# Optimization experiments

Measured on AMD Instinct MI355X. Metric: run time of the kernel, lower is better.

The kernel has to match this reference:

```python
import jax, jax.numpy as jnp
import numpy as np

V, H, HALF, L, B = 32000, 512, 256, 1024, 64
LN_EPS = 1e-5
DELTA_EPS = 1e-6


def _forward(seq, embed, ff_w1, ff_b1, ff_w2, ff_b2, ln_g, ln_b,
             sem_w, sem_b, epi_w, epi_b, out_w, out_b):
    # Encoder: embed -> residual FFN -> LayerNorm
    e = embed[seq]                                   # (B, L, H)
    ff = jax.nn.relu(e @ ff_w1 + ff_b1) @ ff_w2 + ff_b2
    x = e + ff
    mu = jnp.mean(x, axis=-1, keepdims=True)
    var = jnp.mean((x - mu) ** 2, axis=-1, keepdims=True)
    h = (x - mu) / jnp.sqrt(var + LN_EPS) * ln_g + ln_b  # (B, L, H)

    # Project all timesteps at once (batched GEMM instead of per-step Linear)
    ks_all = h @ sem_w + sem_b                       # (B, L, half)
    ke_all = h @ epi_w + epi_b                       # (B, L, half)

    Bsz = seq.shape[0]
    Ls = seq.shape[1]
    w_t = jnp.arange(1, Ls, dtype=h.dtype) / Ls      # (L-1,) linear recency weights

    def step(carry, inp):
        M_s, M_e = carry
        k_s, k_e, w = inp                            # (B, half), (B, half), scalar
        vps = jnp.einsum('bij,bj->bi', M_s, k_s)
        dvs = k_s - vps / (jnp.sum(k_s * k_s, axis=-1, keepdims=True) + DELTA_EPS)
        M_s = M_s + dvs[:, :, None] * k_s[:, None, :]
        vpe = jnp.einsum('bij,bj->bi', M_e, k_e)
        dve = k_e - vpe / (jnp.sum(k_e * k_e, axis=-1, keepdims=True) + DELTA_EPS)
        M_e = M_e + w * (dve[:, :, None] * k_e[:, None, :])
        return (M_s, M_e), None

    M0 = jnp.zeros((Bsz, HALF, HALF), dtype=h.dtype)
    xs = (jnp.swapaxes(ks_all[:, :-1], 0, 1),        # (L-1, B, half)
          jnp.swapaxes(ke_all[:, :-1], 0, 1),
          w_t)
    (M_s, M_e), _ = jax.lax.scan(step, (M0, M0), xs)

    cs = jnp.einsum('bij,bj->bi', M_s, ks_all[:, -1])
    ce = jnp.einsum('bij,bj->bi', M_e, ke_all[:, -1])
    return jnp.concatenate([cs, ce], axis=-1) @ out_w + out_b  # (B, V)


def setup_inputs() -> dict:
    key = jax.random.key(0)
    ks = jax.random.split(key, 8)
    n = lambda k, shape, s=0.02: jax.random.normal(k, shape, jnp.float32) * s
    return {
        'seq': jax.random.randint(ks[0], (B, L), 0, V),
        'embed': n(ks[1], (V, H)),
        'ff_w1': n(ks[2], (H, 2 * H)), 'ff_b1': jnp.zeros((2 * H,), jnp.float32),
        'ff_w2': n(ks[3], (2 * H, H)), 'ff_b2': jnp.zeros((H,), jnp.float32),
        'ln_g': jnp.ones((H,), jnp.float32), 'ln_b': jnp.zeros((H,), jnp.float32),
        'sem_w': n(ks[4], (H, HALF)), 'sem_b': jnp.zeros((HALF,), jnp.float32),
        'epi_w': n(ks[5], (H, HALF)), 'epi_b': jnp.zeros((HALF,), jnp.float32),
        'out_w': n(ks[6], (2 * HALF, V)), 'out_b': jnp.zeros((V,), jnp.float32),
    }


def reference(seq, embed, ff_w1, ff_b1, ff_w2, ff_b2, ln_g, ln_b,
              sem_w, sem_b, epi_w, epi_b, out_w, out_b):
    return _forward(seq, embed, ff_w1, ff_b1, ff_w2, ff_b2, ln_g, ln_b,
                    sem_w, sem_b, epi_w, epi_b, out_w, out_b)
```

## Files before the change

### kernel.cpp

```cpp
#include <hip/hip_runtime.h>

typedef unsigned short ushort_t;
typedef unsigned int uint_t;
typedef __attribute__((ext_vector_type(8))) short short8;
typedef __attribute__((ext_vector_type(4))) float f32x4;

static constexpr int V = 32000, H = 512, HALFD = 256, LSEQ = 1024, BB = 64;

__device__ __forceinline__ ushort_t f2bf(float f) {
    uint_t u = __float_as_uint(f);
    u = (u + 0x7FFFu + ((u >> 16) & 1u)) >> 16;
    return (ushort_t)u;
}
__device__ __forceinline__ float bf2f(ushort_t u) {
    return __uint_as_float(((uint_t)u) << 16);
}
__device__ __forceinline__ float bflo(uint_t u) { return __uint_as_float(u << 16); }
__device__ __forceinline__ float bfhi(uint_t u) { return __uint_as_float(u & 0xffff0000u); }

__global__ void transpose_cvt(const float* __restrict__ W, ushort_t* __restrict__ Wt,
                              int K, int N) {
    __shared__ float tile[32][33];
    int k0 = blockIdx.y * 32, n0 = blockIdx.x * 32;
    int tx = threadIdx.x & 31, ty = threadIdx.x >> 5;
    #pragma unroll
    for (int i = 0; i < 32; i += 8)
        tile[ty + i][tx] = W[(size_t)(k0 + ty + i) * N + n0 + tx];
    __syncthreads();
    #pragma unroll
    for (int i = 0; i < 32; i += 8)
        Wt[(size_t)(n0 + ty + i) * K + k0 + tx] = f2bf(tile[tx][ty + i]);
}

__global__ __launch_bounds__(512) void enc_fused(
        const int* __restrict__ seqp, const float* __restrict__ embed,
        const ushort_t* __restrict__ W1t, const ushort_t* __restrict__ W2t,
        const float* __restrict__ b1, const float* __restrict__ b2,
        const float* __restrict__ lng, const float* __restrict__ lnb,
        const ushort_t* __restrict__ Pt,
        const float* __restrict__ biasS, const float* __restrict__ biasE,
        ushort_t* __restrict__ outS, ushort_t* __restrict__ outE,
        float* __restrict__ bet_s, float* __restrict__ bet_e) {
    __shared__ __align__(16) ushort_t El[64 * 520];
    __shared__ __align__(16) ushort_t T1l[64 * 264];
    __shared__ __align__(16) ushort_t Bst[512 * 40];
    __shared__ int toks[64];
    __shared__ float lnP[64 * 8], lnQ[64 * 8];
    __shared__ float lnM[64], lnR[64];

    int t = threadIdx.x;
    int lane = t & 63, w = t >> 6;
    int lid = lane & 15, quad = lane >> 4;
    int m0 = blockIdx.x * 64;

    if (t < 64) toks[t] = seqp[m0 + t];
    {
        int r = t >> 3, c0 = (t & 7) * 64;
        const float* e = embed + (size_t)seqp[m0 + r] * H + c0;
        #pragma unroll
        for (int j = 0; j < 8; ++j) {
            float4 a = *(const float4*)(e + j * 8);
            float4 bq = *(const float4*)(e + j * 8 + 4);
            short8 sv;
            sv[0] = (short)f2bf(a.x);  sv[1] = (short)f2bf(a.y);
            sv[2] = (short)f2bf(a.z);  sv[3] = (short)f2bf(a.w);
            sv[4] = (short)f2bf(bq.x); sv[5] = (short)f2bf(bq.y);
            sv[6] = (short)f2bf(bq.z); sv[7] = (short)f2bf(bq.w);
            *(short8*)&El[r * 520 + c0 + j * 8] = sv;
        }
    }

    f32x4 acc2[4][4];
    #pragma unroll
    for (int i = 0; i < 4; ++i)
        #pragma unroll
        for (int j = 0; j < 4; ++j)
            acc2[i][j] = (f32x4){0.f, 0.f, 0.f, 0.f};
    __syncthreads();

    for (int s = 0; s < 4; ++s) {
        f32x4 acc1[4][2];
        #pragma unroll
        for (int i = 0; i < 4; ++i)
            #pragma unroll
            for (int j = 0; j < 2; ++j)
                acc1[i][j] = (f32x4){0.f, 0.f, 0.f, 0.f};
        for (int kc = 0; kc < 16; ++kc) {
            {
                int r = t >> 1, ko = (t & 1) * 16;
                const ushort_t* src = W1t + (size_t)(s * 256 + r) * 512 + kc * 32 + ko;
                *(short8*)&Bst[r * 40 + ko]     = *(const short8*)(src);
                *(short8*)&Bst[r * 40 + ko + 8] = *(const short8*)(src + 8);
            }
            __syncthreads();
            short8 af[4], bfr[2];
            #pragma unroll
            for (int i = 0; i < 4; ++i)
                af[i] = *(const short8*)&El[(i * 16 + lid) * 520 + kc * 32 + quad * 8];
            #pragma unroll
            for (int i = 0; i < 2; ++i)
                bfr[i] = *(const short8*)&Bst[(w * 32 + i * 16 + lid) * 40 + quad * 8];
            #pragma unroll
            for (int mt = 0; mt < 4; ++mt)
                #pragma unroll
                for (int nt = 0; nt < 2; ++nt)
                    acc1[mt][nt] = __builtin_amdgcn_mfma_f32_16x16x32_bf16(
                        af[mt], bfr[nt], acc1[mt][nt], 0, 0, 0);
            __syncthreads();
        }
        #pragma unroll
        for (int mt = 0; mt < 4; ++mt)
            #pragma unroll
            for (int nt = 0; nt < 2; ++nt) {
                int col = w * 32 + nt * 16 + lid;
                float bc = b1[s * 256 + col];
                #pragma unroll
                for (int rg = 0; rg < 4; ++rg) {
                    int row = mt * 16 + quad * 4 + rg;
                    T1l[row * 264 + col] = f2bf(fmaxf(acc1[mt][nt][rg] + bc, 0.f));
                }
            }
        for (int kc = 0; kc < 8; ++kc) {
            {
                const ushort_t* src = W2t + (size_t)t * 1024 + s * 256 + kc * 32;
                #pragma unroll
                for (int j = 0; j < 4; ++j)
                    *(short8*)&Bst[t * 40 + j * 8] = *(const short8*)(src + j * 8);
            }
            __syncthreads();
            short8 af[4], bfr[4];
            #pragma unroll
            for (int i = 0; i < 4; ++i)
                af[i] = *(const short8*)&T1l[(i * 16 + lid) * 264 + kc * 32 + quad * 8];
            #pragma unroll
            for (int i = 0; i < 4; ++i)
                bfr[i] = *(const short8*)&Bst[(w * 64 + i * 16 + lid) * 40 + quad * 8];
            #pragma unroll
            for (int mt = 0; mt < 4; ++mt)
                #pragma unroll
                for (int nt = 0; nt < 4; ++nt)
                    acc2[mt][nt] = __builtin_amdgcn_mfma_f32_16x16x32_bf16(
                        af[mt], bfr[nt], acc2[mt][nt], 0, 0, 0);
            __syncthreads();
        }
    }

    #pragma unroll
    for (int mt = 0; mt < 4; ++mt)
        #pragma unroll
        for (int rg = 0; rg < 4; ++rg) {
            int row = mt * 16 + quad * 4 + rg;
            const float* er = embed + (size_t)toks[row] * H;
            #pragma unroll
            for (int nt = 0; nt < 4; ++nt) {
                int col = w * 64 + nt * 16 + lid;
                acc2[mt][nt][rg] += b2[col] + er[col];
            }
        }
    #pragma unroll
    for (int mt = 0; mt < 4; ++mt)
        #pragma unroll
        for (int rg = 0; rg < 4; ++rg) {
            float sv = 0.f, qv = 0.f;
            #pragma unroll
            for (int nt = 0; nt < 4; ++nt) {
                float v = acc2[mt][nt][rg];
                sv += v; qv += v * v;
            }
            #pragma unroll
            for (int d = 1; d < 16; d <<= 1) {
                sv += __shfl_xor(sv, d);
                qv += __shfl_xor(qv, d);
            }
            int row = mt * 16 + quad * 4 + rg;
            if (lid == 0) { lnP[row * 8 + w] = sv; lnQ[row * 8 + w] = qv; }
        }
    __syncthreads();
    if (t < 64) {
        float sv = 0.f, qv = 0.f;
        #pragma unroll
        for (int j = 0; j < 8; ++j) { sv += lnP[t * 8 + j]; qv += lnQ[t * 8 + j]; }
        float mu = sv * (1.f / 512.f);
        float var = qv * (1.f / 512.f) - mu * mu;
        lnM[t] = mu;
        lnR[t] = rsqrtf(var + 1e-5f);
    }
    __syncthreads();
    #pragma unroll
    for (int mt = 0; mt < 4; ++mt)
        #pragma unroll
        for (int rg = 0; rg < 4; ++rg) {
            int row = mt * 16 + quad * 4 + rg;
            float mu = lnM[row], rs = lnR[row];
            #pragma unroll
            for (int nt = 0; nt < 4; ++nt) {
                int col = w * 64 + nt * 16 + lid;
                El[row * 520 + col] =
                    f2bf((acc2[mt][nt][rg] - mu) * rs * lng[col] + lnb[col]);
            }
        }
    __syncthreads();

    f32x4 acc3[4][4];
    #pragma unroll
    for (int i = 0; i < 4; ++i)
        #pragma unroll
        for (int j = 0; j < 4; ++j)
            acc3[i][j] = (f32x4){0.f, 0.f, 0.f, 0.f};
    for (int kc = 0; kc < 16; ++kc) {
        {
            const ushort_t* src = Pt + (size_t)t * 512 + kc * 32;
            #pragma unroll
            for (int j = 0; j < 4; ++j)
                *(short8*)&Bst[t * 40 + j * 8] = *(const short8*)(src + j * 8);
        }
        __syncthreads();
        short8 af[4], bfr[4];
        #pragma unroll
        for (int i = 0; i < 4; ++i)
            af[i] = *(const short8*)&El[(i * 16 + lid) * 520 + kc * 32 + quad * 8];
        #pragma unroll
        for (int i = 0; i < 4; ++i)
            bfr[i] = *(const short8*)&Bst[(w * 64 + i * 16 + lid) * 40 + quad * 8];
        #pragma unroll
        for (int mt = 0; mt < 4; ++mt)
            #pragma unroll
            for (int nt = 0; nt < 4; ++nt)
                acc3[mt][nt] = __builtin_amdgcn_mfma_f32_16x16x32_bf16(
                    af[mt], bfr[nt], acc3[mt][nt], 0, 0, 0);
        __syncthreads();
    }
    {
        const float* bb = (w < 4) ? (biasS + w * 64) : (biasE + (w - 4) * 64);
        ushort_t* op = (w < 4) ? outS : outE;
        int cbase = (w < 4) ? (w * 64) : ((w - 4) * 64);
        #pragma unroll
        for (int mt = 0; mt < 4; ++mt)
            #pragma unroll
            for (int rg = 0; rg < 4; ++rg) {
                int row = mt * 16 + quad * 4 + rg;
                float sq = 0.f;
                #pragma unroll
                for (int nt = 0; nt < 4; ++nt) {
                    int c = nt * 16 + lid;
                    ushort_t hv = f2bf(acc3[mt][nt][rg] + bb[c]);
                    op[(size_t)(m0 + row) * HALFD + cbase + c] = hv;
                    float fv = bf2f(hv);
                    sq += fv * fv;
                }
                #pragma unroll
                for (int d = 1; d < 16; d <<= 1) sq += __shfl_xor(sq, d);
                if (lid == 0) lnP[row * 8 + w] = sq;
            }
        __syncthreads();
        if (t < 128) {
            int row = t & 63;
            int w0 = (t < 64) ? 0 : 4;
            float sv = lnP[row * 8 + w0] + lnP[row * 8 + w0 + 1]
                     + lnP[row * 8 + w0 + 2] + lnP[row * 8 + w0 + 3];
            float* bout = (t < 64) ? bet_s : bet_e;
            bout[m0 + row] = sv + 1e-6f;
        }
    }
}

__global__ __launch_bounds__(256) void tinv_kernel(
        const ushort_t* __restrict__ ks, const ushort_t* __restrict__ ke,
        const float* __restrict__ beta_s, const float* __restrict__ beta_e,
        ushort_t* __restrict__ Dg) {
    __shared__ __align__(16) ushort_t Kl[64][280];
    __shared__ __align__(16) ushort_t LmT[4][64][66];
    __shared__ float betsl[4][64];

    int t = threadIdx.x;
    int lane = t & 63, wv = t >> 6;
    int lid = lane & 15, quad = lane >> 4;
    int blk0 = blockIdx.x * 4;
    const float invL = 1.0f / 1024.0f;

    for (int pp = 0; pp < 4; ++pp) {
        int p = blk0 + pp;
        int ch = p & 15, bm = p >> 4;
        int mat = bm & 1, b = bm >> 1;
        const ushort_t* Kp = (mat ? ke : ks) + ((size_t)b * LSEQ + ch * 64) * HALFD;
        const float* Bp = (mat ? beta_e : beta_s) + (size_t)b * LSEQ + ch * 64;

        __syncthreads();
        {
            int j = t >> 2, c0 = (t & 3) * 64;
            const ushort_t* src = Kp + (size_t)j * HALFD + c0;
            #pragma unroll
            for (int x = 0; x < 8; ++x)
                *(short8*)&Kl[j][c0 + x * 8] = *(const short8*)(src + x * 8);
        }
        if (t < 64) betsl[pp][t] = Bp[t];
        __syncthreads();

        f32x4 g[4];
        #pragma unroll
        for (int i = 0; i < 4; ++i) g[i] = (f32x4){0.f, 0.f, 0.f, 0.f};
        #pragma unroll
        for (int kc = 0; kc < 8; ++kc) {
            short8 af = *(const short8*)&Kl[wv * 16 + lid][kc * 32 + quad * 8];
            #pragma unroll
            for (int nt = 0; nt < 4; ++nt) {
                short8 bq = *(const short8*)&Kl[nt * 16 + lid][kc * 32 + quad * 8];
                g[nt] = __builtin_amdgcn_mfma_f32_16x16x32_bf16(af, bq, g[nt], 0, 0, 0);
            }
        }
        #pragma unroll
        for (int nt = 0; nt < 4; ++nt)
            #pragma unroll
            for (int rg = 0; rg < 4; ++rg) {
                int i = wv * 16 + quad * 4 + rg;
                int j = nt * 16 + lid;
                int s = ch * 64 + i;
                float wgt = mat ? (float)(s + 1) * invL : 1.0f;
                if (s >= 1023) wgt = 0.f;
                float wb = wgt / betsl[pp][i];
                LmT[pp][j][i] = f2bf((j < i) ? g[nt][rg] * wb : 0.f);
            }
    }
    __syncthreads();

    const ushort_t (*Lp)[66] = LmT[wv];
    float a[64];
    #pragma unroll
    for (int x = 0; x < 32; ++x) {
        uint_t u = *(const uint_t*)&Lp[lane][x * 2];
        a[x * 2]     = -bflo(u);
        a[x * 2 + 1] = -bfhi(u);
    }
    #pragma unroll
    for (int j = 0; j < 63; ++j) {
        float dj = a[j];
        const ushort_t* rowj = Lp[j];
        #pragma unroll
        for (int ii = (j + 1) & ~1; ii < 64; ii += 2) {
            uint_t u = *(const uint_t*)&rowj[ii];
            if (ii > j) a[ii] -= bflo(u) * dj;
            a[ii + 1]        -= bfhi(u) * dj;
        }
    }
    size_t pbase = (size_t)(blk0 + wv) * 4096;
    #pragma unroll
    for (int i = 0; i < 64; ++i)
        Dg[pbase + (size_t)i * 64 + lane] = f2bf(a[i]);
}

__global__ __launch_bounds__(512) void scan_kernel(
        const ushort_t* __restrict__ ks, const ushort_t* __restrict__ ke,
        const float* __restrict__ beta_s, const float* __restrict__ beta_e,
        const ushort_t* __restrict__ Dg, float* __restrict__ c) {
    int blk = blockIdx.x;
    int b = blk >> 2, mat = (blk >> 1) & 1, half = blk & 1;
    const ushort_t* Kp = (mat ? ke : ks) + (size_t)b * LSEQ * HALFD;
    const float* Bp = (mat ? beta_e : beta_s) + (size_t)b * LSEQ;
    const ushort_t* Dp = Dg + (size_t)(b * 2 + mat) * 16 * 4096;

    __shared__ __align__(16) ushort_t Kl[64][264];
    __shared__ __align__(16) ushort_t MK[33792];
    __shared__ __align__(16) ushort_t RHSl[128][72];
    __shared__ __align__(16) ushort_t Ul[128][72];
    __shared__ __align__(16) ushort_t Dl[64][72];
    __shared__ float bets[LSEQ];

    ushort_t (*Ml)[264] = (ushort_t(*)[264])MK;
    ushort_t (*Kt)[72]  = (ushort_t(*)[72])MK;

    int t = threadIdx.x;
    int lane = t & 63, wid = t >> 6;
    int lid = lane & 15, quad = lane >> 4;
    int wm  = (wid & 1) * 64, wn  = (wid >> 1) * 64;
    int wm1 = (wid & 1) * 64, wn1 = (wid >> 1) * 16;

    #pragma unroll
    for (int i = 0; i < 2; ++i) bets[t + i * 512] = Bp[t + i * 512];

    f32x4 acc[4][4];
    #pragma unroll
    for (int i = 0; i < 4; ++i)
        #pragma unroll
        for (int j = 0; j < 4; ++j)
            acc[i][j] = (f32x4){0.f, 0.f, 0.f, 0.f};

    int sj = t >> 3, scb = (t & 7) * 8;
    short8 pf[4];
    {
        const ushort_t* kr = Kp + (size_t)sj * HALFD + scb;
        #pragma unroll
        for (int x = 0; x < 4; ++x) pf[x] = *(const short8*)(kr + x * 64);
    }
    short8 dpf = *(const short8*)(Dp + t * 8);
    const float invL = 1.0f / 1024.0f;

    for (int ch = 0; ch < 16; ++ch) {
        __syncthreads();
        #pragma unroll
        for (int x = 0; x < 4; ++x) *(short8*)&Kl[sj][scb + x * 64] = pf[x];
        *(short8*)&Dl[t >> 3][(t & 7) * 8] = dpf;
        #pragma unroll
        for (int mt = 0; mt < 4; ++mt)
            #pragma unroll
            for (int nt = 0; nt < 4; ++nt)
                #pragma unroll
                for (int rg = 0; rg < 4; ++rg)
                    Ml[wm + mt * 16 + quad * 4 + rg][wn + nt * 16 + lid] =
                        f2bf(acc[mt][nt][rg]);
        int nch = (ch + 1 < 16) ? ch + 1 : 15;
        {
            const ushort_t* kr = Kp + ((size_t)nch * 64 + sj) * HALFD + scb;
            #pragma unroll
            for (int x = 0; x < 4; ++x) pf[x] = *(const short8*)(kr + x * 64);
            dpf = *(const short8*)(Dp + (size_t)nch * 4096 + t * 8);
        }
        __syncthreads();

        f32x4 p0[4];
        #pragma unroll
        for (int i = 0; i < 4; ++i) p0[i] = (f32x4){0.f, 0.f, 0.f, 0.f};
        #pragma unroll
        for (int kc = 0; kc < 8; ++kc) {
            short8 bq = *(const short8*)&Kl[wn1 + lid][kc * 32 + quad * 8];
            #pragma unroll
            for (int mt = 0; mt < 4; ++mt) {
                short8 aq = *(const short8*)&Ml[wm1 + mt * 16 + lid][kc * 32 + quad * 8];
                p0[mt] = __builtin_amdgcn_mfma_f32_16x16x32_bf16(aq, bq, p0[mt], 0, 0, 0);
            }
        }
        __syncthreads();
        #pragma unroll
        for (int mt = 0; mt < 4; ++mt)
            #pragma unroll
            for (int nt = 0; nt < 4; ++nt)
                #pragma unroll
                for (int rg = 0; rg < 4; ++rg) {
                    float v = acc[mt][nt][rg];
                    Ml[wm + mt * 16 + quad * 4 + rg][wn + nt * 16 + lid] =
                        f2bf(v - bf2f(f2bf(v)));
                }
        __syncthreads();
        #pragma unroll
        for (int kc = 0; kc < 8; ++kc) {
            short8 bq = *(const short8*)&Kl[wn1 + lid][kc * 32 + quad * 8];
            #pragma unroll
            for (int mt = 0; mt < 4; ++mt) {
                short8 aq = *(const short8*)&Ml[wm1 + mt * 16 + lid][kc * 32 + quad * 8];
                p0[mt] = __builtin_amdgcn_mfma_f32_16x16x32_bf16(aq, bq, p0[mt], 0, 0, 0);
            }
        }
        int iB = wn1 + lid;
        int s = ch * 64 + iB;
        float wgt = mat ? (float)(s + 1) * invL : 1.0f;
        if (s >= 1023) wgt = 0.f;
        float wb = wgt / bets[s];
        float rhsf[4][4];
        #pragma unroll
        for (int mt = 0; mt < 4; ++mt)
            #pragma unroll
            for (int rg = 0; rg < 4; ++rg) {
                int r = wm1 + mt * 16 + quad * 4 + rg;
                float kv = bf2f(Kl[iB][half * 128 + r]);
                float rv = wgt * kv - wb * p0[mt][rg];
                rhsf[mt][rg] = rv;
                RHSl[r][iB] = f2bf(rv);
            }
        __syncthreads();

        {
            int c0 = wid * 32;
            #pragma unroll
            for (int rr = 0; rr < 4; ++rr) {
                short8 kv8 = *(const short8*)&Kl[lane][c0 + rr * 8];
                #pragma unroll
                for (int x = 0; x < 8; ++x)
                    Kt[c0 + rr * 8 + x][lane] = (ushort_t)kv8[x];
            }
        }
        f32x4 uf[4];
        #pragma unroll
        for (int i = 0; i < 4; ++i) uf[i] = (f32x4){0.f, 0.f, 0.f, 0.f};
        #pragma unroll
        for (int kc = 0; kc < 2; ++kc) {
            short8 bq = *(const short8*)&Dl[wn1 + lid][kc * 32 + quad * 8];
            #pragma unroll
            for (int mt = 0; mt < 4; ++mt) {
                short8 aq = *(const short8*)&RHSl[wm1 + mt * 16 + lid][kc * 32 + quad * 8];
                uf[mt] = __builtin_amdgcn_mfma_f32_16x16x32_bf16(aq, bq, uf[mt], 0, 0, 0);
            }
        }
        #pragma unroll
        for (int mt = 0; mt < 4; ++mt)
            #pragma unroll
            for (int rg = 0; rg < 4; ++rg) {
                int r = wm1 + mt * 16 + quad * 4 + rg;
                Ul[r][wn1 + lid] = f2bf(uf[mt][rg] + rhsf[mt][rg]);
            }
        __syncthreads();
        #pragma unroll
        for (int kc = 0; kc < 2; ++kc) {
            short8 bq4[4];
            #pragma unroll
            for (int nt = 0; nt < 4; ++nt)
                bq4[nt] = *(const short8*)&Kt[wn + nt * 16 + lid][kc * 32 + quad * 8];
            #pragma unroll
            for (int mt = 0; mt < 4; ++mt) {
                short8 aq = *(const short8*)&Ul[wm + mt * 16 + lid][kc * 32 + quad * 8];
                #pragma unroll
                for (int nt = 0; nt < 4; ++nt)
                    acc[mt][nt] = __builtin_amdgcn_mfma_f32_16x16x32_bf16(
                        aq, bq4[nt], acc[mt][nt], 0, 0, 0);
            }
        }
        __syncthreads();
        #pragma unroll
        for (int mt = 0; mt < 4; ++mt)
            #pragma unroll
            for (int rg = 0; rg < 4; ++rg) {
                int r = wm1 + mt * 16 + quad * 4 + rg;
                float u = uf[mt][rg] + rhsf[mt][rg];
                Ul[r][wn1 + lid] = f2bf(u - bf2f(f2bf(u)));
            }
        __syncthreads();
        #pragma unroll
        for (int kc = 0; kc < 2; ++kc) {
            short8 bq4[4];
            #pragma unroll
            for (int nt = 0; nt < 4; ++nt)
                bq4[nt] = *(const short8*)&Kt[wn + nt * 16 + lid][kc * 32 + quad * 8];
            #pragma unroll
            for (int mt = 0; mt < 4; ++mt) {
                short8 aq = *(const short8*)&Ul[wm + mt * 16 + lid][kc * 32 + quad * 8];
                #pragma unroll
                for (int nt = 0; nt < 4; ++nt)
                    acc[mt][nt] = __builtin_amdgcn_mfma_f32_16x16x32_bf16(
                        aq, bq4[nt], acc[mt][nt], 0, 0, 0);
            }
        }
    }

    __syncthreads();
    float* vsc = (float*)RHSl;
    float kvv[4];
    #pragma unroll
    for (int nt = 0; nt < 4; ++nt)
        kvv[nt] = bf2f(Kl[63][wn + nt * 16 + lid]);
    #pragma unroll
    for (int mt = 0; mt < 4; ++mt)
        #pragma unroll
        for (int rg = 0; rg < 4; ++rg) {
            float p = acc[mt][0][rg] * kvv[0] + acc[mt][1][rg] * kvv[1]
                    + acc[mt][2][rg] * kvv[2] + acc[mt][3][rg] * kvv[3];
            p += __shfl_xor(p, 1); p += __shfl_xor(p, 2);
            p += __shfl_xor(p, 4); p += __shfl_xor(p, 8);
            if (lid == 0)
                vsc[(wid >> 1) * 128 + wm + mt * 16 + quad * 4 + rg] = p;
        }
    __syncthreads();
    if (t < 128) {
        float sum = vsc[t] + vsc[128 + t] + vsc[256 + t] + vsc[384 + t];
        c[(size_t)b * 512 + mat * 256 + half * 128 + t] = sum;
    }
}

__global__ __launch_bounds__(512) void out_gemm(
        const float* __restrict__ c, const float* __restrict__ W,
        const float* __restrict__ bias, float* __restrict__ out) {
    __shared__ __align__(16) float cl[16][512];
    int t = threadIdx.x;
    int lane = t & 63, w = t >> 6;
    int cb = blockIdx.x * 256;
    int rb = blockIdx.y * 16;

    #pragma unroll
    for (int i = 0; i < 4; ++i) {
        int idx = t + i * 512;
        int row = idx >> 7, c4 = (idx & 127) * 4;
        *(float4*)&cl[row][c4] = *(const float4*)(c + (size_t)(rb + row) * 512 + c4);
    }
    __syncthreads();

    const float* wp = W + cb + lane * 4;
    int r0 = w * 2;
    f32x4 a0 = (f32x4){0.f, 0.f, 0.f, 0.f};
    f32x4 a1 = (f32x4){0.f, 0.f, 0.f, 0.f};

    #pragma unroll 2
    for (int k = 0; k < 512; k += 4) {
        f32x4 w0 = *(const f32x4*)(wp + (size_t)(k + 0) * V);
        f32x4 w1 = *(const f32x4*)(wp + (size_t)(k + 1) * V);
        f32x4 w2 = *(const f32x4*)(wp + (size_t)(k + 2) * V);
        f32x4 w3 = *(const f32x4*)(wp + (size_t)(k + 3) * V);
        f32x4 ca = *(const f32x4*)&cl[r0][k];
        f32x4 cb4 = *(const f32x4*)&cl[r0 + 1][k];
        a0 += ca[0] * w0; a0 += ca[1] * w1; a0 += ca[2] * w2; a0 += ca[3] * w3;
        a1 += cb4[0] * w0; a1 += cb4[1] * w1; a1 += cb4[2] * w2; a1 += cb4[3] * w3;
    }
    f32x4 bv = *(const f32x4*)(bias + cb + lane * 4);
    *(f32x4*)(out + (size_t)(rb + r0) * V + cb + lane * 4) = a0 + bv;
    *(f32x4*)(out + (size_t)(rb + r0 + 1) * V + cb + lane * 4) = a1 + bv;
}

extern "C" void kernel_launch(void* const* d_in, const int* in_sizes, int n_in,
                              void* d_out, int out_size, void* d_ws, size_t ws_size,
                              hipStream_t stream) {
    const int*   seq    = (const int*)d_in[0];
    const float* embed  = (const float*)d_in[1];
    const float* ff_w1  = (const float*)d_in[2];
    const float* ff_b1  = (const float*)d_in[3];
    const float* ff_w2  = (const float*)d_in[4];
    const float* ff_b2  = (const float*)d_in[5];
    const float* ln_g   = (const float*)d_in[6];
    const float* ln_b   = (const float*)d_in[7];
    const float* sem_w  = (const float*)d_in[8];
    const float* sem_b  = (const float*)d_in[9];
    const float* epi_w  = (const float*)d_in[10];
    const float* epi_b  = (const float*)d_in[11];
    const float* out_w  = (const float*)d_in[12];
    const float* out_b  = (const float*)d_in[13];
    float* outp = (float*)d_out;

    char* w = (char*)d_ws;
    size_t off = 0;
    ushort_t* ks_bf = (ushort_t*)(w + off); off += 33554432;
    ushort_t* ke_bf = (ushort_t*)(w + off); off += 33554432;
    ushort_t* w1t   = (ushort_t*)(w + off); off += 1048576;
    ushort_t* w2t   = (ushort_t*)(w + off); off += 1048576;
    ushort_t* semt  = (ushort_t*)(w + off); off += 262144;
    ushort_t* epit  = (ushort_t*)(w + off); off += 262144;
    float*    bet_s = (float*)(w + off);    off += 262144;
    float*    bet_e = (float*)(w + off);    off += 262144;
    float*    cbuf  = (float*)(w + off);    off += 131072;
    ushort_t* Dbuf  = (ushort_t*)(w + off); off += 16777216;

    transpose_cvt<<<dim3(1024 / 32, 512 / 32), 256, 0, stream>>>(ff_w1, w1t, 512, 1024);
    transpose_cvt<<<dim3(512 / 32, 1024 / 32), 256, 0, stream>>>(ff_w2, w2t, 1024, 512);
    transpose_cvt<<<dim3(256 / 32, 512 / 32), 256, 0, stream>>>(sem_w, semt, 512, 256);
    transpose_cvt<<<dim3(256 / 32, 512 / 32), 256, 0, stream>>>(epi_w, epit, 512, 256);

    enc_fused<<<1024, 512, 0, stream>>>(
        seq, embed, w1t, w2t, ff_b1, ff_b2, ln_g, ln_b,
        semt, sem_b, epi_b, ks_bf, ke_bf, bet_s, bet_e);

    tinv_kernel<<<512, 256, 0, stream>>>(ks_bf, ke_bf, bet_s, bet_e, Dbuf);
    scan_kernel<<<256, 512, 0, stream>>>(ks_bf, ke_bf, bet_s, bet_e, Dbuf, cbuf);

    out_gemm<<<dim3(125, 4), 512, 0, stream>>>(cbuf, out_w, out_b, outp);
}
```

Measured before the change: 962.6 us.

## Load encoder GEMM B-fragments directly from global into registers with prefetch

In the fused encoder kernel, all three GEMM stages stop staging weight tiles through a shared-memory buffer with two barriers per k-chunk. Each wave now loads its own B fragments straight from global memory into registers and prefetches the next k-chunk while issuing the MFMAs. This removes the shared buffer and most block-wide syncs, which lowers LDS use and may raise occupancy. The cost is more register pressure and uncoalesced global loads that depend on L2/cache reuse across blocks.

```diff
diff --git a/kernel.cpp b/kernel.cpp
--- a/kernel.cpp
+++ b/kernel.cpp
@@ -43,7 +43,6 @@
         float* __restrict__ bet_s, float* __restrict__ bet_e) {
     __shared__ __align__(16) ushort_t El[64 * 520];
     __shared__ __align__(16) ushort_t T1l[64 * 264];
-    __shared__ __align__(16) ushort_t Bst[512 * 40];
     __shared__ int toks[64];
     __shared__ float lnP[64 * 8], lnQ[64 * 8];
     __shared__ float lnM[64], lnR[64];
@@ -85,28 +84,29 @@
             #pragma unroll
             for (int j = 0; j < 2; ++j)
                 acc1[i][j] = (f32x4){0.f, 0.f, 0.f, 0.f};
-        for (int kc = 0; kc < 16; ++kc) {
-            {
-                int r = t >> 1, ko = (t & 1) * 16;
-                const ushort_t* src = W1t + (size_t)(s * 256 + r) * 512 + kc * 32 + ko;
-                *(short8*)&Bst[r * 40 + ko]     = *(const short8*)(src);
-                *(short8*)&Bst[r * 40 + ko + 8] = *(const short8*)(src + 8);
-            }
-            __syncthreads();
-            short8 af[4], bfr[2];
-            #pragma unroll
-            for (int i = 0; i < 4; ++i)
-                af[i] = *(const short8*)&El[(i * 16 + lid) * 520 + kc * 32 + quad * 8];
-            #pragma unroll
-            for (int i = 0; i < 2; ++i)
-                bfr[i] = *(const short8*)&Bst[(w * 32 + i * 16 + lid) * 40 + quad * 8];
-            #pragma unroll
-            for (int mt = 0; mt < 4; ++mt)
-                #pragma unroll
-                for (int nt = 0; nt < 2; ++nt)
-                    acc1[mt][nt] = __builtin_amdgcn_mfma_f32_16x16x32_bf16(
-                        af[mt], bfr[nt], acc1[mt][nt], 0, 0, 0);
-            __syncthreads();
+        {
+            const ushort_t* wb = W1t + (size_t)(s * 256 + w * 32 + lid) * 512 + quad * 8;
+            short8 bc0 = *(const short8*)(wb);
+            short8 bc1 = *(const short8*)(wb + 16 * 512);
+            for (int kc = 0; kc < 16; ++kc) {
+                short8 bn0 = bc0, bn1 = bc1;
+                if (kc < 15) {
+                    bn0 = *(const short8*)(wb + (kc + 1) * 32);
+                    bn1 = *(const short8*)(wb + 16 * 512 + (kc + 1) * 32);
+                }
+                short8 af[4];
+                #pragma unroll
+                for (int i = 0; i < 4; ++i)
+                    af[i] = *(const short8*)&El[(i * 16 + lid) * 520 + kc * 32 + quad * 8];
+                #pragma unroll
+                for (int mt = 0; mt < 4; ++mt) {
+                    acc1[mt][0] = __builtin_amdgcn_mfma_f32_16x16x32_bf16(
+                        af[mt], bc0, acc1[mt][0], 0, 0, 0);
+                    acc1[mt][1] = __builtin_amdgcn_mfma_f32_16x16x32_bf16(
+                        af[mt], bc1, acc1[mt][1], 0, 0, 0);
+                }
+                bc0 = bn0; bc1 = bn1;
+            }
         }
         #pragma unroll
         for (int mt = 0; mt < 4; ++mt)
@@ -120,29 +120,41 @@
                     T1l[row * 264 + col] = f2bf(fmaxf(acc1[mt][nt][rg] + bc, 0.f));
                 }
             }
-        for (int kc = 0; kc < 8; ++kc) {
-            {
-                const ushort_t* src = W2t + (size_t)t * 1024 + s * 256 + kc * 32;
-                #pragma unroll
-                for (int j = 0; j < 4; ++j)
-                    *(short8*)&Bst[t * 40 + j * 8] = *(const short8*)(src + j * 8);
-            }
-            __syncthreads();
-            short8 af[4], bfr[4];
-            #pragma unroll
-            for (int i = 0; i < 4; ++i)
-                af[i] = *(const short8*)&T1l[(i * 16 + lid) * 264 + kc * 32 + quad * 8];
-            #pragma unroll
-            for (int i = 0; i < 4; ++i)
-                bfr[i] = *(const short8*)&Bst[(w * 64 + i * 16 + lid) * 40 + quad * 8];
-            #pragma unroll
-            for (int mt = 0; mt < 4; ++mt)
-                #pragma unroll
-                for (int nt = 0; nt < 4; ++nt)
-                    acc2[mt][nt] = __builtin_amdgcn_mfma_f32_16x16x32_bf16(
-                        af[mt], bfr[nt], acc2[mt][nt], 0, 0, 0);
-            __syncthreads();
-        }
+        __syncthreads();
+
+        {
+            const ushort_t* wb = W2t + (size_t)(w * 64 + lid) * 1024 + s * 256 + quad * 8;
+            short8 bc0 = *(const short8*)(wb);
+            short8 bc1 = *(const short8*)(wb + 16 * 1024);
+            short8 bc2 = *(const short8*)(wb + 32 * 1024);
+            short8 bc3 = *(const short8*)(wb + 48 * 1024);
+            for (int kc = 0; kc < 8; ++kc) {
+                short8 bn0 = bc0, bn1 = bc1, bn2 = bc2, bn3 = bc3;
+                if (kc < 7) {
+                    bn0 = *(const short8*)(wb + (kc + 1) * 32);
+                    bn1 = *(const short8*)(wb + 16 * 1024 + (kc + 1) * 32);
+                    bn2 = *(const short8*)(wb + 32 * 1024 + (kc + 1) * 32);
+                    bn3 = *(const short8*)(wb + 48 * 1024 + (kc + 1) * 32);
+                }
+                short8 af[4];
+                #pragma unroll
+                for (int i = 0; i < 4; ++i)
+                    af[i] = *(const short8*)&T1l[(i * 16 + lid) * 264 + kc * 32 + quad * 8];
+                #pragma unroll
+                for (int mt = 0; mt < 4; ++mt) {
+                    acc2[mt][0] = __builtin_amdgcn_mfma_f32_16x16x32_bf16(
+                        af[mt], bc0, acc2[mt][0], 0, 0, 0);
+                    acc2[mt][1] = __builtin_amdgcn_mfma_f32_16x16x32_bf16(
+                        af[mt], bc1, acc2[mt][1], 0, 0, 0);
+                    acc2[mt][2] = __builtin_amdgcn_mfma_f32_16x16x32_bf16(
+                        af[mt], bc2, acc2[mt][2], 0, 0, 0);
+                    acc2[mt][3] = __builtin_amdgcn_mfma_f32_16x16x32_bf16(
+                        af[mt], bc3, acc2[mt][3], 0, 0, 0);
+                }
+                bc0 = bn0; bc1 = bn1; bc2 = bn2; bc3 = bn3;
+            }
+        }
+        __syncthreads();
     }
 
     #pragma unroll
@@ -207,28 +219,37 @@
         #pragma unroll
         for (int j = 0; j < 4; ++j)
             acc3[i][j] = (f32x4){0.f, 0.f, 0.f, 0.f};
-    for (int kc = 0; kc < 16; ++kc) {
-        {
-            const ushort_t* src = Pt + (size_t)t * 512 + kc * 32;
-            #pragma unroll
-            for (int j = 0; j < 4; ++j)
-                *(short8*)&Bst[t * 40 + j * 8] = *(const short8*)(src + j * 8);
-        }
-        __syncthreads();
-        short8 af[4], bfr[4];
-        #pragma unroll
-        for (int i = 0; i < 4; ++i)
-            af[i] = *(const short8*)&El[(i * 16 + lid) * 520 + kc * 32 + quad * 8];
-        #pragma unroll
-        for (int i = 0; i < 4; ++i)
-            bfr[i] = *(const short8*)&Bst[(w * 64 + i * 16 + lid) * 40 + quad * 8];
-        #pragma unroll
-        for (int mt = 0; mt < 4; ++mt)
-            #pragma unroll
-            for (int nt = 0; nt < 4; ++nt)
-                acc3[mt][nt] = __builtin_amdgcn_mfma_f32_16x16x32_bf16(
-                    af[mt], bfr[nt], acc3[mt][nt], 0, 0, 0);
-        __syncthreads();
+    {
+        const ushort_t* pb = Pt + (size_t)(w * 64 + lid) * 512 + quad * 8;
+        short8 bc0 = *(const short8*)(pb);
+        short8 bc1 = *(const short8*)(pb + 16 * 512);
+        short8 bc2 = *(const short8*)(pb + 32 * 512);
+        short8 bc3 = *(const short8*)(pb + 48 * 512);
+        for (int kc = 0; kc < 16; ++kc) {
+            short8 bn0 = bc0, bn1 = bc1, bn2 = bc2, bn3 = bc3;
+            if (kc < 15) {
+                bn0 = *(const short8*)(pb + (kc + 1) * 32);
+                bn1 = *(const short8*)(pb + 16 * 512 + (kc + 1) * 32);
+                bn2 = *(const short8*)(pb + 32 * 512 + (kc + 1) * 32);
+                bn3 = *(const short8*)(pb + 48 * 512 + (kc + 1) * 32);
+            }
+            short8 af[4];
+            #pragma unroll
+            for (int i = 0; i < 4; ++i)
+                af[i] = *(const short8*)&El[(i * 16 + lid) * 520 + kc * 32 + quad * 8];
+            #pragma unroll
+            for (int mt = 0; mt < 4; ++mt) {
+                acc3[mt][0] = __builtin_amdgcn_mfma_f32_16x16x32_bf16(
+                    af[mt], bc0, acc3[mt][0], 0, 0, 0);
+                acc3[mt][1] = __builtin_amdgcn_mfma_f32_16x16x32_bf16(
+                    af[mt], bc1, acc3[mt][1], 0, 0, 0);
+                acc3[mt][2] = __builtin_amdgcn_mfma_f32_16x16x32_bf16(
+                    af[mt], bc2, acc3[mt][2], 0, 0, 0);
+                acc3[mt][3] = __builtin_amdgcn_mfma_f32_16x16x32_bf16(
+                    af[mt], bc3, acc3[mt][3], 0, 0, 0);
+            }
+            bc0 = bn0; bc1 = bn1; bc2 = bn2; bc3 = bn3;
+        }
     }
     {
         const float* bb = (w < 4) ? (biasS + w * 64) : (biasE + (w - 4) * 64);
```

Result: faster. 818.4 us (-15.0%).
